# Optimization experiments

Hardware: AMD Instinct MI355X
Metric: run time of the kernel (lower is better)

## Reference

```python
import jax, jax.numpy as jnp
import numpy as np

H = 2048          # hidden_size
L_CACHE = 3       # depthwise conv kernel size
BATCH, SEQ = 2, 4096


def setup_inputs() -> dict:
    key = jax.random.key(0)
    k1, k2, k3, k4 = jax.random.split(key, 4)
    hidden_states = jax.random.normal(k1, (BATCH, SEQ, H), dtype=jnp.float32)
    # torch nn.Linear weights: [out_features, in_features]
    W_in = jax.random.normal(k2, (3 * H, H), dtype=jnp.float32) * (1.0 / np.sqrt(H))
    W_out = jax.random.normal(k3, (H, H), dtype=jnp.float32) * (1.0 / np.sqrt(H))
    # torch depthwise Conv1d weight: [H, 1, L]
    W_conv = jax.random.normal(k4, (H, 1, L_CACHE), dtype=jnp.float32) * (1.0 / np.sqrt(L_CACHE))
    return {"hidden_states": hidden_states, "W_in": W_in, "W_conv": W_conv, "W_out": W_out}


def reference(hidden_states, W_in, W_conv, W_out):
    # in_proj: [B,S,H] @ [H,3H] -> [B,S,3H]
    BCx = jnp.einsum('bsh,oh->bso', hidden_states, W_in)
    Bg, Cg, x = jnp.split(BCx, 3, axis=-1)   # each [B,S,H]
    Bx = Bg * x                              # gate before conv
    # depthwise causal conv over sequence: operate in NCH layout
    Bx_nch = jnp.transpose(Bx, (0, 2, 1))    # [B,H,S]
    conv_out = jax.lax.conv_general_dilated(
        Bx_nch, W_conv,
        window_strides=(1,),
        padding=[(L_CACHE - 1, 0)],          # causal: left pad only
        dimension_numbers=('NCH', 'OIH', 'NCH'),
        feature_group_count=H,
    )                                        # [B,H,S]
    y = Cg * jnp.transpose(conv_out, (0, 2, 1))  # C gating, back to [B,S,H]
    return jnp.einsum('bsh,oh->bso', y, W_out)   # out_proj
```

## Files before the change

### kernel.cpp

```cpp
#include <hip/hip_runtime.h>
#include <hip/hip_fp16.h>


typedef _Float16 f16x8 __attribute__((ext_vector_type(8)));
typedef float    f32x4 __attribute__((ext_vector_type(4)));

#define GLD_LDS16(gsrc, sdst) \
  __builtin_amdgcn_global_load_lds((const __attribute__((address_space(1))) void*)(gsrc), \
                                   (__attribute__((address_space(3))) void*)(sdst), 16, 0, 0)

#define VMCNT4 asm volatile("s_waitcnt vmcnt(4)" ::: "memory")
#define VMCNT0 asm volatile("s_waitcnt vmcnt(0)" ::: "memory")
#define LGKM0  asm volatile("s_waitcnt lgkmcnt(0)" ::: "memory")
#define BAR    __builtin_amdgcn_s_barrier()
#define FENCE  asm volatile("" ::: "memory")

__global__ __launch_bounds__(256) void cvt_all(const float* __restrict__ X,
                                               const float* __restrict__ Wi,
                                               const float* __restrict__ Wo,
                                               _Float16* __restrict__ Xh,
                                               _Float16* __restrict__ Wih,
                                               _Float16* __restrict__ Woh) {
  int base = (blockIdx.x * 256 + threadIdx.x) * 8;
  const float* src;
  _Float16* dst;
  if (base < 16777216) {
    src = X + base; dst = Xh + base;
  } else if (base < 29360128) {
    int off = base - 16777216;
    int row = off >> 11, col = off & 2047;
    int rd = (row < 2048) ? (row << 1) : (row < 4096 ? row + 2048 : (((row - 4096) << 1) | 1));
    src = Wi + off; dst = Wih + rd * 2048 + col;
  } else {
    int off = base - 29360128;
    src = Wo + off; dst = Woh + off;
  }
  const float4* p = reinterpret_cast<const float4*>(src);
  float4 a = p[0], b = p[1];
  f16x8 o;
  o[0] = (_Float16)a.x; o[1] = (_Float16)a.y; o[2] = (_Float16)a.z; o[3] = (_Float16)a.w;
  o[4] = (_Float16)b.x; o[5] = (_Float16)b.y; o[6] = (_Float16)b.z; o[7] = (_Float16)b.w;
  *reinterpret_cast<f16x8*>(dst) = o;
}

__global__ __launch_bounds__(256) void conv_gate2(const _Float16* __restrict__ Bx,
                                                  const _Float16* __restrict__ Cgb,
                                                  const float* __restrict__ Wc,
                                                  _Float16* __restrict__ Y) {
  const int h0 = threadIdx.x * 8;
  const int r0 = blockIdx.x * 8;
  const int s0 = r0 & 4095;

  float w0[8], w1[8], w2[8];
#pragma unroll
  for (int j = 0; j < 8; ++j) {
    w0[j] = Wc[(h0 + j) * 3 + 0];
    w1[j] = Wc[(h0 + j) * 3 + 1];
    w2[j] = Wc[(h0 + j) * 3 + 2];
  }

  float bxm2[8] = {}, bxm1[8] = {};
  if (s0 != 0) {
    f16x8 b2 = *reinterpret_cast<const f16x8*>(Bx + (size_t)(r0 - 2) * 2048 + h0);
    f16x8 b1 = *reinterpret_cast<const f16x8*>(Bx + (size_t)(r0 - 1) * 2048 + h0);
#pragma unroll
    for (int j = 0; j < 8; ++j) { bxm2[j] = (float)b2[j]; bxm1[j] = (float)b1[j]; }
  }

  for (int i = 0; i < 8; ++i) {
    f16x8 bxv = *reinterpret_cast<const f16x8*>(Bx  + (size_t)(r0 + i) * 2048 + h0);
    f16x8 cgv = *reinterpret_cast<const f16x8*>(Cgb + (size_t)(r0 + i) * 2048 + h0);
    f16x8 o;
#pragma unroll
    for (int j = 0; j < 8; ++j) {
      float bx   = (float)bxv[j];
      float conv = w0[j] * bxm2[j] + w1[j] * bxm1[j] + w2[j] * bx;
      o[j] = (_Float16)((float)cgv[j] * conv);
      bxm2[j] = bxm1[j];
      bxm1[j] = bx;
    }
    *reinterpret_cast<f16x8*>(Y + (size_t)(r0 + i) * 2048 + h0) = o;
  }
}

__device__ __forceinline__ void ldA(f16x8 (&af)[4][2], const _Float16* p, int base, int ak0, int ak1) {
#pragma unroll
  for (int i = 0; i < 4; ++i) {
    af[i][0] = *(const f16x8*)(p + base + i * 1024 + ak0);
    af[i][1] = *(const f16x8*)(p + base + i * 1024 + ak1);
  }
}
__device__ __forceinline__ void ldB(f16x8 (&bf)[2][2], const _Float16* p, int base, int ak0, int ak1) {
#pragma unroll
  for (int j = 0; j < 2; ++j) {
    bf[j][0] = *(const f16x8*)(p + base + j * 1024 + ak0);
    bf[j][1] = *(const f16x8*)(p + base + j * 1024 + ak1);
  }
}
template <int QM, int QN>
__device__ __forceinline__ void mfmaQ(f32x4 (&acc)[8][4], const f16x8 (&af)[4][2], const f16x8 (&bf)[2][2]) {
  __builtin_amdgcn_s_setprio(1);
#pragma unroll
  for (int i = 0; i < 4; ++i)
#pragma unroll
    for (int j = 0; j < 2; ++j)
#pragma unroll
      for (int ks = 0; ks < 2; ++ks)
        acc[QM * 4 + i][QN * 2 + j] =
            __builtin_amdgcn_mfma_f32_16x16x32_f16(af[i][ks], bf[j][ks], acc[QM * 4 + i][QN * 2 + j], 0, 0, 0);
  __builtin_amdgcn_s_setprio(0);
}

template <typename CT, int MODE>
__global__ __launch_bounds__(512, 2) void gemm8p(const _Float16* __restrict__ Ag,
                                                 const _Float16* __restrict__ Bg,
                                                 CT* __restrict__ Cg_out,
                                                 _Float16* __restrict__ BxP,
                                                 _Float16* __restrict__ CgP,
                                                 int N, int K) {
  __shared__ __align__(16) char smem[131072];
  const int tid = threadIdx.x, lane = tid & 63, w = tid >> 6;
  const int wr = w >> 2, wc = w & 3;

  const int xcd = (int)blockIdx.x & 7;
  const int i4  = (int)blockIdx.x >> 3;
  const int bm = (((xcd << 2) + ((i4 & 31) >> 3))) << 8;
  const int bn = ((((i4 >> 5) << 3)) + (i4 & 7)) << 8;

  _Float16* const A0 = (_Float16*)(smem);
  _Float16* const B0 = (_Float16*)(smem + 32768);
  _Float16* const A1 = (_Float16*)(smem + 65536);
  _Float16* const B1 = (_Float16*)(smem + 98304);

  const int rr = tid >> 3;
  const int sCol = ((tid & 7) ^ (rr & 7)) * 8;
  const _Float16* aSrc = Ag + (size_t)(bm + rr) * K + sCol;
  const _Float16* bSrc = Bg + (size_t)(bn + (rr >> 5) * 64 + (rr & 31)) * K + sCol;

  const int ak0 = ((lane >> 4) ^ (lane & 7)) * 8;
  const int ak1 = (((lane >> 4) + 4) ^ (lane & 7)) * 8;
  const int aRB = (wr * 128 + (lane & 15)) * 64;
  const int bRB = (wc * 32 + (lane & 15)) * 64;

  const int nt = K >> 6;

#define STG_A(NBO, kt, u) GLD_LDS16(aSrc + (size_t)(u) * 64 * K + (kt) * 64, \
                                    smem + (NBO) + (u) * 8192 + tid * 16)
#define STG_B(NBO, kt, u) GLD_LDS16(bSrc + (size_t)(((u) & 1) * 128 + ((u) >> 1) * 32) * K + (kt) * 64, \
                                    smem + (NBO) + 32768 + (u) * 8192 + tid * 16)

  f16x8 af[4][2], bf[2][2];
  f32x4 acc[8][4] = {};

  STG_A(0, 0, 0); STG_A(0, 0, 2);
  STG_B(0, 0, 0); STG_B(0, 0, 1);
  STG_B(0, 0, 2); STG_B(0, 0, 3);
  STG_A(0, 0, 1); STG_A(0, 0, 3);
  VMCNT4; BAR; FENCE;

#define TILE(AB, BB, NBO, t)                                       \
  {                                                                \
    const int tn = ((t) + 1 < nt) ? (t) + 1 : nt - 1;              \
    ldA(af, AB, aRB, ak0, ak1);                                    \
    ldB(bf, BB, bRB, ak0, ak1);                                    \
    STG_A(NBO, tn, 0); STG_A(NBO, tn, 2);                          \
    VMCNT4; BAR; FENCE;                                            \
    mfmaQ<0, 0>(acc, af, bf);                                      \
    ldB(bf, BB, bRB + 8192, ak0, ak1);                             \
    STG_B(NBO, tn, 0); STG_B(NBO, tn, 1);                          \
    VMCNT4; BAR; FENCE;                                            \
    mfmaQ<0, 1>(acc, af, bf);                                      \
    ldA(af, AB, aRB + 4096, ak0, ak1);                             \
    STG_B(NBO, tn, 2); STG_B(NBO, tn, 3);                          \
    BAR; FENCE;                                                    \
    mfmaQ<1, 1>(acc, af, bf);                                      \
    ldB(bf, BB, bRB, ak0, ak1);                                    \
    STG_A(NBO, tn, 1); STG_A(NBO, tn, 3);                          \
    VMCNT4; BAR; FENCE;                                            \
    mfmaQ<1, 0>(acc, af, bf);                                      \
  }

  for (int t = 0; t < nt; t += 2) {
    TILE(A0, B0, 65536, t);
    TILE(A1, B1, 0, t + 1);
  }
  LGKM0; VMCNT0;

  const int rb  = bm + wr * 128 + ((lane >> 4) << 2);
  const int cbl = bn + wc * 64 + (lane & 15);
  if (MODE == 0) {
#pragma unroll
    for (int mi = 0; mi < 8; ++mi)
#pragma unroll
      for (int nj = 0; nj < 4; ++nj) {
        f32x4 v = acc[mi][nj];
#pragma unroll
        for (int rg = 0; rg < 4; ++rg)
          Cg_out[(size_t)(rb + mi * 16 + rg) * N + cbl + nj * 16] = (CT)v[rg];
      }
  } else if (bn < 4096) {
    const bool writer = ((lane & 1) == 0);
#pragma unroll
    for (int mi = 0; mi < 8; ++mi)
#pragma unroll
      for (int nj = 0; nj < 4; ++nj) {
        f32x4 v = acc[mi][nj];
        const int h = (cbl + nj * 16) >> 1;
#pragma unroll
        for (int rg = 0; rg < 4; ++rg) {
          float part = __shfl_xor(v[rg], 1);
          float p = v[rg] * part;
          if (writer)
            BxP[(size_t)(rb + mi * 16 + rg) * 2048 + h] = (_Float16)p;
        }
      }
  } else {
    const int hc = cbl - 4096;
#pragma unroll
    for (int mi = 0; mi < 8; ++mi)
#pragma unroll
      for (int nj = 0; nj < 4; ++nj) {
        f32x4 v = acc[mi][nj];
#pragma unroll
        for (int rg = 0; rg < 4; ++rg)
          CgP[(size_t)(rb + mi * 16 + rg) * 2048 + hc + nj * 16] = (_Float16)v[rg];
      }
  }
#undef TILE
#undef STG_A
#undef STG_B
}

extern "C" void kernel_launch(void* const* d_in, const int* in_sizes, int n_in,
                              void* d_out, int out_size, void* d_ws, size_t ws_size,
                              hipStream_t stream) {
  const float* X  = (const float*)d_in[0];
  const float* Wi = (const float*)d_in[1];
  const float* Wc = (const float*)d_in[2];
  const float* Wo = (const float*)d_in[3];
  float* out = (float*)d_out;

  char* ws = (char*)d_ws;
  _Float16* Xh  = (_Float16*)(ws);
  _Float16* Wih = (_Float16*)(ws + 33554432);
  _Float16* Woh = (_Float16*)(ws + 58720256);
  _Float16* Bx  = (_Float16*)(ws + 67108864);
  _Float16* CgB = (_Float16*)(ws + 100663296);
  _Float16* Yh  = (_Float16*)(ws + 134217728);
  (void)ws_size; (void)in_sizes; (void)n_in; (void)out_size;

  cvt_all<<<dim3(16384), 256, 0, stream>>>(X, Wi, Wo, Xh, Wih, Woh);

  gemm8p<_Float16, 1><<<dim3(768), 512, 0, stream>>>(Xh, Wih, Bx, Bx, CgB, 6144, 2048);

  conv_gate2<<<dim3(1024), 256, 0, stream>>>(Bx, CgB, Wc, Yh);

  gemm8p<float, 0><<<dim3(256), 512, 0, stream>>>(Yh, Woh, out, nullptr, nullptr, 2048, 2048);
}
```

Before: 290.2 us.

## Make in_proj GEMM persistent over three N tiles with cross-tile prefetch

The in_proj GEMM now launches 256 blocks, and each block loops over three output column tiles instead of launching 768 single-tile blocks. The last k-step of one tile prefetches the first k-slice of the next tile's B operand, so the pipeline never drains between tiles. The A rows stay fixed per block, which may improve L2 reuse. In exchange, the epilogue stores for one tile now sit serially inside the loop, and the grid is smaller, so any load imbalance or tail effect is concentrated in fewer blocks.

```diff
diff --git a/kernel.cpp b/kernel.cpp
--- a/kernel.cpp
+++ b/kernel.cpp
@@ -111,7 +111,7 @@
   __builtin_amdgcn_s_setprio(0);
 }
 
-template <typename CT, int MODE>
+template <typename CT, int MODE, int OT>
 __global__ __launch_bounds__(512, 2) void gemm8p(const _Float16* __restrict__ Ag,
                                                  const _Float16* __restrict__ Bg,
                                                  CT* __restrict__ Cg_out,
@@ -124,8 +124,8 @@
 
   const int xcd = (int)blockIdx.x & 7;
   const int i4  = (int)blockIdx.x >> 3;
-  const int bm = (((xcd << 2) + ((i4 & 31) >> 3))) << 8;
-  const int bn = ((((i4 >> 5) << 3)) + (i4 & 7)) << 8;
+  const int bm  = ((xcd << 2) + (i4 >> 3)) << 8;
+  const int bn0 = i4 & 7;
 
   _Float16* const A0 = (_Float16*)(smem);
   _Float16* const B0 = (_Float16*)(smem + 32768);
@@ -135,7 +135,7 @@
   const int rr = tid >> 3;
   const int sCol = ((tid & 7) ^ (rr & 7)) * 8;
   const _Float16* aSrc = Ag + (size_t)(bm + rr) * K + sCol;
-  const _Float16* bSrc = Bg + (size_t)(bn + (rr >> 5) * 64 + (rr & 31)) * K + sCol;
+  const size_t bRowOff = (size_t)((rr >> 5) * 64 + (rr & 31)) * K + sCol;
 
   const int ak0 = ((lane >> 4) ^ (lane & 7)) * 8;
   const int ak1 = (((lane >> 4) + 4) ^ (lane & 7)) * 8;
@@ -146,86 +146,105 @@
 
 #define STG_A(NBO, kt, u) GLD_LDS16(aSrc + (size_t)(u) * 64 * K + (kt) * 64, \
                                     smem + (NBO) + (u) * 8192 + tid * 16)
-#define STG_B(NBO, kt, u) GLD_LDS16(bSrc + (size_t)(((u) & 1) * 128 + ((u) >> 1) * 32) * K + (kt) * 64, \
-                                    smem + (NBO) + 32768 + (u) * 8192 + tid * 16)
+#define STG_B(NBO, kt, u, BS) GLD_LDS16((BS) + (size_t)(((u) & 1) * 128 + ((u) >> 1) * 32) * K + (kt) * 64, \
+                                        smem + (NBO) + 32768 + (u) * 8192 + tid * 16)
 
   f16x8 af[4][2], bf[2][2];
   f32x4 acc[8][4] = {};
 
-  STG_A(0, 0, 0); STG_A(0, 0, 2);
-  STG_B(0, 0, 0); STG_B(0, 0, 1);
-  STG_B(0, 0, 2); STG_B(0, 0, 3);
-  STG_A(0, 0, 1); STG_A(0, 0, 3);
-  VMCNT4; BAR; FENCE;
-
-#define TILE(AB, BB, NBO, t)                                       \
+  {
+    const _Float16* b0src = Bg + (size_t)(bn0 << 8) * K + bRowOff;
+    STG_A(0, 0, 0); STG_A(0, 0, 2);
+    STG_B(0, 0, 0, b0src); STG_B(0, 0, 1, b0src);
+    STG_B(0, 0, 2, b0src); STG_B(0, 0, 3, b0src);
+    STG_A(0, 0, 1); STG_A(0, 0, 3);
+    VMCNT4; BAR; FENCE;
+  }
+
+#define TILE(AB, BB, NBO, ktS, bS)                                 \
   {                                                                \
-    const int tn = ((t) + 1 < nt) ? (t) + 1 : nt - 1;              \
     ldA(af, AB, aRB, ak0, ak1);                                    \
     ldB(bf, BB, bRB, ak0, ak1);                                    \
-    STG_A(NBO, tn, 0); STG_A(NBO, tn, 2);                          \
+    STG_A(NBO, ktS, 0); STG_A(NBO, ktS, 2);                        \
     VMCNT4; BAR; FENCE;                                            \
     mfmaQ<0, 0>(acc, af, bf);                                      \
     ldB(bf, BB, bRB + 8192, ak0, ak1);                             \
-    STG_B(NBO, tn, 0); STG_B(NBO, tn, 1);                          \
+    STG_B(NBO, ktS, 0, bS); STG_B(NBO, ktS, 1, bS);                \
     VMCNT4; BAR; FENCE;                                            \
     mfmaQ<0, 1>(acc, af, bf);                                      \
     ldA(af, AB, aRB + 4096, ak0, ak1);                             \
-    STG_B(NBO, tn, 2); STG_B(NBO, tn, 3);                          \
+    STG_B(NBO, ktS, 2, bS); STG_B(NBO, ktS, 3, bS);                \
     BAR; FENCE;                                                    \
     mfmaQ<1, 1>(acc, af, bf);                                      \
     ldB(bf, BB, bRB, ak0, ak1);                                    \
-    STG_A(NBO, tn, 1); STG_A(NBO, tn, 3);                          \
+    STG_A(NBO, ktS, 1); STG_A(NBO, ktS, 3);                        \
     VMCNT4; BAR; FENCE;                                            \
     mfmaQ<1, 0>(acc, af, bf);                                      \
   }
 
-  for (int t = 0; t < nt; t += 2) {
-    TILE(A0, B0, 65536, t);
-    TILE(A1, B1, 0, t + 1);
+  for (int ot = 0; ot < OT; ++ot) {
+    const int bn  = ((ot << 3) + bn0) << 8;
+    const int bnN = (ot + 1 < OT) ? (((ot + 1) << 3) + bn0) << 8 : bn;
+    const _Float16* bSrcC = Bg + (size_t)bn * K + bRowOff;
+    const _Float16* bSrcN = Bg + (size_t)bnN * K + bRowOff;
+
+    for (int t = 0; t < nt; t += 2) {
+      TILE(A0, B0, 65536, t + 1, bSrcC);
+      const bool wrap = (t + 2 >= nt);
+      const _Float16* bs2 = wrap ? bSrcN : bSrcC;
+      const int kt2 = wrap ? 0 : t + 2;
+      TILE(A1, B1, 0, kt2, bs2);
+    }
+
+    const int rb  = bm + wr * 128 + ((lane >> 4) << 2);
+    const int cbl = bn + wc * 64 + (lane & 15);
+    if (MODE == 0) {
+#pragma unroll
+      for (int mi = 0; mi < 8; ++mi)
+#pragma unroll
+        for (int nj = 0; nj < 4; ++nj) {
+          f32x4 v = acc[mi][nj];
+#pragma unroll
+          for (int rg = 0; rg < 4; ++rg)
+            Cg_out[(size_t)(rb + mi * 16 + rg) * N + cbl + nj * 16] = (CT)v[rg];
+        }
+    } else if (bn < 4096) {
+      const bool writer = ((lane & 1) == 0);
+#pragma unroll
+      for (int mi = 0; mi < 8; ++mi)
+#pragma unroll
+        for (int nj = 0; nj < 4; ++nj) {
+          f32x4 v = acc[mi][nj];
+          const int h = (cbl + nj * 16) >> 1;
+#pragma unroll
+          for (int rg = 0; rg < 4; ++rg) {
+            float part = __shfl_xor(v[rg], 1);
+            float p = v[rg] * part;
+            if (writer)
+              BxP[(size_t)(rb + mi * 16 + rg) * 2048 + h] = (_Float16)p;
+          }
+        }
+    } else {
+      const int hc = cbl - 4096;
+#pragma unroll
+      for (int mi = 0; mi < 8; ++mi)
+#pragma unroll
+        for (int nj = 0; nj < 4; ++nj) {
+          f32x4 v = acc[mi][nj];
+#pragma unroll
+          for (int rg = 0; rg < 4; ++rg)
+            CgP[(size_t)(rb + mi * 16 + rg) * 2048 + hc + nj * 16] = (_Float16)v[rg];
+        }
+    }
+    if (ot + 1 < OT) {
+#pragma unroll
+      for (int mi = 0; mi < 8; ++mi)
+#pragma unroll
+        for (int nj = 0; nj < 4; ++nj)
+          acc[mi][nj] = (f32x4)0.0f;
+    }
   }
   LGKM0; VMCNT0;
-
-  const int rb  = bm + wr * 128 + ((lane >> 4) << 2);
-  const int cbl = bn + wc * 64 + (lane & 15);
-  if (MODE == 0) {
-#pragma unroll
-    for (int mi = 0; mi < 8; ++mi)
-#pragma unroll
-      for (int nj = 0; nj < 4; ++nj) {
-        f32x4 v = acc[mi][nj];
-#pragma unroll
-        for (int rg = 0; rg < 4; ++rg)
-          Cg_out[(size_t)(rb + mi * 16 + rg) * N + cbl + nj * 16] = (CT)v[rg];
-      }
-  } else if (bn < 4096) {
-    const bool writer = ((lane & 1) == 0);
-#pragma unroll
-    for (int mi = 0; mi < 8; ++mi)
-#pragma unroll
-      for (int nj = 0; nj < 4; ++nj) {
-        f32x4 v = acc[mi][nj];
-        const int h = (cbl + nj * 16) >> 1;
-#pragma unroll
-        for (int rg = 0; rg < 4; ++rg) {
-          float part = __shfl_xor(v[rg], 1);
-          float p = v[rg] * part;
-          if (writer)
-            BxP[(size_t)(rb + mi * 16 + rg) * 2048 + h] = (_Float16)p;
-        }
-      }
-  } else {
-    const int hc = cbl - 4096;
-#pragma unroll
-    for (int mi = 0; mi < 8; ++mi)
-#pragma unroll
-      for (int nj = 0; nj < 4; ++nj) {
-        f32x4 v = acc[mi][nj];
-#pragma unroll
-        for (int rg = 0; rg < 4; ++rg)
-          CgP[(size_t)(rb + mi * 16 + rg) * 2048 + hc + nj * 16] = (_Float16)v[rg];
-      }
-  }
 #undef TILE
 #undef STG_A
 #undef STG_B
@@ -251,9 +270,9 @@
 
   cvt_all<<<dim3(16384), 256, 0, stream>>>(X, Wi, Wo, Xh, Wih, Woh);
 
-  gemm8p<_Float16, 1><<<dim3(768), 512, 0, stream>>>(Xh, Wih, Bx, Bx, CgB, 6144, 2048);
+  gemm8p<_Float16, 1, 3><<<dim3(256), 512, 0, stream>>>(Xh, Wih, Bx, Bx, CgB, 6144, 2048);
 
   conv_gate2<<<dim3(1024), 256, 0, stream>>>(Bx, CgB, Wc, Yh);
 
-  gemm8p<float, 0><<<dim3(256), 512, 0, stream>>>(Yh, Woh, out, nullptr, nullptr, 2048, 2048);
-}
+  gemm8p<float, 0, 1><<<dim3(256), 512, 0, stream>>>(Yh, Woh, out, nullptr, nullptr, 2048, 2048);
+}
```

New measurement: 301.2 us. +3.8%, slower.
